# Performance work log

Hardware: AMD Instinct MI355X
Metric: run time of the kernel (lower is better)

## Reference

```python
import jax, jax.numpy as jnp
import numpy as np

K, B, S, D, V, H = 4, 64, 50, 256, 40000, 4
DH = D // H
TOPK = 2
NEG = -1e9
SCALE = float(1.0 / np.sqrt(DH))


def setup_inputs() -> dict:
    key = jax.random.key(0)
    ks = jax.random.split(key, 16)
    s = 0.05
    return {
        "ids":   jax.random.randint(ks[0], (K, B, S), 0, V),
        "items": jax.random.randint(ks[1], (K, B, S), 0, V),
        "adj":   jax.random.randint(ks[2], (B, S, S), 0, 5),
        "alias": jax.random.randint(ks[3], (B, S), 0, S),
        "eps":   jax.random.normal(ks[4], (B, S, K), jnp.float32),
        "emb":   jax.random.normal(ks[5], (K, V, D), jnp.float32) * s,
        "agg_a": jax.random.normal(ks[6], (K, 4, D), jnp.float32) * s,
        "Wq": jax.random.normal(ks[7], (K, D, D), jnp.float32) * s,
        "Wk": jax.random.normal(ks[8], (K, D, D), jnp.float32) * s,
        "Wv": jax.random.normal(ks[9], (K, D, D), jnp.float32) * s,
        "Wo": jax.random.normal(ks[10], (K, D, D), jnp.float32) * s,
        "ln1_g": jnp.ones((K, D), jnp.float32),
        "ln1_b": jnp.zeros((K, D), jnp.float32),
        "W1": jax.random.normal(ks[11], (K, D, 4 * D), jnp.float32) * s,
        "W2": jax.random.normal(ks[12], (K, 4 * D, D), jnp.float32) * s,
        "ln2_g": jnp.ones((K, D), jnp.float32),
        "ln2_b": jnp.zeros((K, D), jnp.float32),
        "Wg": jax.random.normal(ks[13], (D, K), jnp.float32) * s,
        "Wn": jax.random.normal(ks[14], (D, K), jnp.float32) * s,
    }


def _layer_norm(x, g, b):
    m = jnp.mean(x, -1, keepdims=True)
    v = jnp.var(x, -1, keepdims=True)
    return (x - m) * jax.lax.rsqrt(v + 1e-5) * g + b


def _per_key(ids, items, emb, a, Wq, Wk, Wv, Wo, g1, b1, W1, W2, g2, b2, adj, alias):
    hg = emb[items]                                          # [B,S,D] graph-node embeddings
    # LocalAggregator: relation-typed pairwise attention over session graph (adj in {1..4})
    e = jnp.einsum('bid,bjd,rd->rbij', hg, hg, a)            # [4,B,S,S], avoids [B,S,S,D]
    e = jax.nn.leaky_relu(e, 0.2)
    alpha = jnp.full(adj.shape, NEG, e.dtype)
    for r in range(4):
        alpha = jnp.where(adj == r + 1, e[r], alpha)
    alpha = jax.nn.softmax(alpha, -1)
    h_local = jnp.einsum('bij,bjd->bid', alpha, hg)          # graph aggregation
    h = jnp.take_along_axis(h_local, alias[..., None], axis=1)   # distribute graph rows to sequence
    # memory-transformer block (pre-LN causal MHA + FFN)
    x = _layer_norm(h, g1, b1)
    q = (x @ Wq).reshape(B, S, H, DH)
    k = (x @ Wk).reshape(B, S, H, DH)
    v = (x @ Wv).reshape(B, S, H, DH)
    scores = jnp.einsum('bihd,bjhd->bhij', q, k) * SCALE
    causal = jnp.tril(jnp.ones((S, S), bool))
    scores = jnp.where(causal, scores, NEG)
    attn = jax.nn.softmax(scores, -1)
    o = jnp.einsum('bhij,bjhd->bihd', attn, v).reshape(B, S, D) @ Wo
    h = h + o
    y = _layer_norm(h, g2, b2)
    h = h + jax.nn.gelu(y @ W1) @ W2
    return h


def reference(ids, items, adj, alias, eps, emb, agg_a, Wq, Wk, Wv, Wo,
              ln1_g, ln1_b, W1, W2, ln2_g, ln2_b, Wg, Wn):
    per_key = jax.vmap(_per_key, in_axes=(0,) * 14 + (None, None))
    h_keys = per_key(ids, items, emb, agg_a, Wq, Wk, Wv, Wo,
                     ln1_g, ln1_b, W1, W2, ln2_g, ln2_b, adj, alias)   # [K,B,S,D]
    # gate input: mean over per-key input-sequence embeddings (h_seq in original)
    h_seq = jax.vmap(lambda e, i: e[i])(emb, ids).mean(0)              # [B,S,D]
    # noisy top-k gating over node-type experts
    logits = h_seq @ Wg + jax.nn.softplus(h_seq @ Wn) * eps            # [B,S,K]
    top_v, top_i = jax.lax.top_k(logits, TOPK)
    w = jax.nn.softmax(top_v, -1)                                      # [B,S,TOPK]
    gates = jnp.sum(jax.nn.one_hot(top_i, K, dtype=w.dtype) * w[..., None], axis=-2)  # [B,S,K]
    return jnp.einsum('bsk,kbsd->bsd', gates, h_keys)
```

## Files before the change

kernel.cpp:

```cpp
#include <hip/hip_runtime.h>
#include <hip/hip_bf16.h>
#include <math.h>

#define K_ 4
#define B_ 64
#define S_ 50
#define D_ 256
#define V_ 40000
#define H_ 4
#define DH_ 64
#define NEG_ (-1e9f)
#define SCALE_ 0.125f

typedef __attribute__((ext_vector_type(8))) __bf16 bf16x8v;
typedef __attribute__((ext_vector_type(4))) float f32x4v;

__device__ __forceinline__ float wred_sum(float v) {
#pragma unroll
  for (int off = 32; off > 0; off >>= 1) v += __shfl_xor(v, off, 64);
  return v;
}
__device__ __forceinline__ float wred_max(float v) {
#pragma unroll
  for (int off = 32; off > 0; off >>= 1) v = fmaxf(v, __shfl_xor(v, off, 64));
  return v;
}
__device__ __forceinline__ float softplusf(float x) {
  return (x > 20.f) ? x : log1pf(expf(x));
}
__device__ __forceinline__ float geluf(float x) {
  const float c = 0.7978845608028654f;
  float x3 = x * x * x;
  return 0.5f * x * (1.f + tanhf(c * (x + 0.044715f * x3)));
}
__device__ __forceinline__ float bf2f(unsigned int u) {
  return __uint_as_float(u << 16);
}
__device__ __forceinline__ unsigned short f2bf(float f) {
  unsigned u = __float_as_uint(f);
  return (unsigned short)((u + 0x7fffu + ((u >> 16) & 1u)) >> 16);
}
__device__ __forceinline__ void unp8(uint4 a, float* d) {
  d[0] = bf2f(a.x & 0xffffu); d[1] = bf2f(a.x >> 16);
  d[2] = bf2f(a.y & 0xffffu); d[3] = bf2f(a.y >> 16);
  d[4] = bf2f(a.z & 0xffffu); d[5] = bf2f(a.z >> 16);
  d[6] = bf2f(a.w & 0xffffu); d[7] = bf2f(a.w >> 16);
}
__device__ __forceinline__ bf16x8v cvt8(float4 a, float4 b) {
  bf16x8v r;
  r[0] = (__bf16)a.x; r[1] = (__bf16)a.y; r[2] = (__bf16)a.z; r[3] = (__bf16)a.w;
  r[4] = (__bf16)b.x; r[5] = (__bf16)b.y; r[6] = (__bf16)b.z; r[7] = (__bf16)b.w;
  return r;
}

__global__ __launch_bounds__(256) void front_kernel(
    const int* __restrict__ items, const int* __restrict__ adj,
    const float* __restrict__ emb, const float* __restrict__ agg_a,
    const int* __restrict__ alias_, float* __restrict__ hbuf,
    unsigned short* __restrict__ xb,
    const float* __restrict__ ln1g, const float* __restrict__ ln1b,
    const int* __restrict__ ids, const float* __restrict__ Wg,
    const float* __restrict__ Wn, const float* __restrict__ eps,
    float* __restrict__ gates,
    const float* __restrict__ wq, const float* __restrict__ wk,
    const float* __restrict__ wv, const float* __restrict__ wo,
    const float* __restrict__ w1, const float* __restrict__ w2,
    unsigned short* __restrict__ wqkvT, unsigned short* __restrict__ woT,
    unsigned short* __restrict__ w1T, unsigned short* __restrict__ w2T) {
  __shared__ __align__(16) char smem[62816];
  int bid = blockIdx.x;
  int t = threadIdx.x;

  if (bid < 256) {
    typedef __bf16 (*arr264)[264];
    arr264 hgb = (arr264)smem;
    float (*e_f)[68] = (float(*)[68])(smem + 33792);
    unsigned char (*adj_s)[64] = (unsigned char(*)[64])(smem + 47392);
    arr264 a_sb = (arr264)(smem + 51488);
    __bf16 (*alp)[72] = (__bf16(*)[72])(smem + 53600);
    float* hl = (float*)smem;

    int kb = bid;
    int k = kb >> 6, b = kb & 63;
    for (int c = t; c < 2048; c += 256) {
      int row = c >> 5, c8 = (c & 31) * 8;
      bf16x8v val;
      if (row < S_) {
        int g = items[kb * S_ + row];
        const float* src = emb + ((long)k * V_ + g) * D_ + c8;
        val = cvt8(*(const float4*)src, *(const float4*)(src + 4));
      } else {
#pragma unroll
        for (int e = 0; e < 8; ++e) val[e] = (__bf16)0.f;
      }
      *(bf16x8v*)&hgb[row][c8] = val;
    }
    if (t < 128) {
      int row = t >> 5, c8 = (t & 31) * 8;
      const float* src = agg_a + ((long)k * 4 + row) * D_ + c8;
      *(bf16x8v*)&a_sb[row][c8] = cvt8(*(const float4*)src, *(const float4*)(src + 4));
    }
    for (int c = t; c < 4096; c += 256) {
      int i = c >> 6, j = c & 63;
      adj_s[i][j] = (i < S_ && j < S_)
                        ? (unsigned char)adj[((long)b * S_ + i) * S_ + j] : 0;
    }
    __syncthreads();
    int w = t >> 6, lane = t & 63;
    int m16 = lane & 15, quad = lane >> 4;
    float e_sel[4][4];
#pragma unroll
    for (int nt = 0; nt < 4; ++nt)
#pragma unroll
      for (int rg = 0; rg < 4; ++rg) e_sel[nt][rg] = NEG_;
#pragma unroll
    for (int r = 0; r < 4; ++r) {
      f32x4v acc[4];
#pragma unroll
      for (int nt = 0; nt < 4; ++nt) acc[nt] = (f32x4v){0.f, 0.f, 0.f, 0.f};
#pragma unroll
      for (int k0 = 0; k0 < 8; ++k0) {
        int kc = k0 * 32 + quad * 8;
        bf16x8v hr = *(const bf16x8v*)&hgb[w * 16 + m16][kc];
        bf16x8v ar = *(const bf16x8v*)&a_sb[r][kc];
        bf16x8v af;
#pragma unroll
        for (int e = 0; e < 8; ++e) af[e] = (__bf16)((float)hr[e] * (float)ar[e]);
#pragma unroll
        for (int nt = 0; nt < 4; ++nt) {
          bf16x8v bf = *(const bf16x8v*)&hgb[nt * 16 + m16][kc];
          acc[nt] = __builtin_amdgcn_mfma_f32_16x16x32_bf16(af, bf, acc[nt], 0, 0, 0);
        }
      }
#pragma unroll
      for (int nt = 0; nt < 4; ++nt)
#pragma unroll
        for (int rg = 0; rg < 4; ++rg) {
          int i = w * 16 + quad * 4 + rg, j = nt * 16 + m16;
          if (adj_s[i][j] == r + 1) {
            float v = acc[nt][rg];
            e_sel[nt][rg] = (v >= 0.f) ? v : 0.2f * v;
          }
        }
    }
#pragma unroll
    for (int nt = 0; nt < 4; ++nt)
#pragma unroll
      for (int rg = 0; rg < 4; ++rg) {
        int i = w * 16 + quad * 4 + rg;
        if (i < S_) e_f[i][nt * 16 + m16] = e_sel[nt][rg];
      }
    __syncthreads();
    for (int i = w; i < S_; i += 4) {
      float val = (lane < S_) ? e_f[i][lane] : -INFINITY;
      float m = wred_max(val);
      float p = expf(val - m);
      float ssum = wred_sum(p);
      alp[i][lane] = (__bf16)(p / ssum);
    }
    __syncthreads();
    f32x4v acc16[16];
#pragma unroll
    for (int nt = 0; nt < 16; ++nt) {
      f32x4v acc = (f32x4v){0.f, 0.f, 0.f, 0.f};
#pragma unroll
      for (int k0 = 0; k0 < 2; ++k0) {
        int jb = k0 * 32 + quad * 8;
        bf16x8v af = *(const bf16x8v*)&alp[w * 16 + m16][jb];
        bf16x8v bf;
#pragma unroll
        for (int tt = 0; tt < 8; ++tt) bf[tt] = hgb[jb + tt][nt * 16 + m16];
        acc = __builtin_amdgcn_mfma_f32_16x16x32_bf16(af, bf, acc, 0, 0, 0);
      }
      acc16[nt] = acc;
    }
    __syncthreads();
#pragma unroll
    for (int nt = 0; nt < 16; ++nt)
#pragma unroll
      for (int rg = 0; rg < 4; ++rg) {
        int i = w * 16 + quad * 4 + rg;
        if (i < S_) hl[i * 260 + nt * 16 + m16] = acc16[nt][rg];
      }
    __syncthreads();
    for (int s = w; s < S_; s += 4) {
      int src = alias_[b * S_ + s];
      const float4 v = *(const float4*)&hl[src * 260 + lane * 4];
      long off = ((long)kb * S_ + s) * D_ + lane * 4;
      *(float4*)(hbuf + off) = v;
      float sum = wred_sum(v.x + v.y + v.z + v.w);
      float sq = wred_sum(v.x * v.x + v.y * v.y + v.z * v.z + v.w * v.w);
      float mean = sum * (1.f / D_);
      float var = sq * (1.f / D_) - mean * mean;
      float rs = rsqrtf(var + 1e-5f);
      const float4 gv = *(const float4*)(ln1g + k * D_ + lane * 4);
      const float4 bv = *(const float4*)(ln1b + k * D_ + lane * 4);
      ushort4 o;
      o.x = f2bf((v.x - mean) * rs * gv.x + bv.x);
      o.y = f2bf((v.y - mean) * rs * gv.y + bv.y);
      o.z = f2bf((v.z - mean) * rs * gv.z + bv.z);
      o.w = f2bf((v.w - mean) * rs * gv.w + bv.w);
      *(ushort4*)(xb + off) = o;
    }
    return;
  }

  if (bid < 1024) {
    int tid = bid - 256;
    typedef unsigned short row66[66];
    row66* tile = (row66*)smem;
    const float* src; unsigned short* dst; int C, R; int r0, c0;
    if (tid < 192) {
      int sect = tid >> 6; int rem = tid & 63;
      int k = rem >> 4, t2 = rem & 15;
      r0 = (t2 >> 2) * 64; c0 = (t2 & 3) * 64;
      src = ((sect == 0) ? wq : (sect == 1) ? wk : wv) + (long)k * 65536;
      dst = wqkvT + ((long)k * 768 + sect * 256) * 256;
      R = 256; C = 256;
    } else if (tid < 256) {
      int rem = tid - 192; int k = rem >> 4, t2 = rem & 15;
      r0 = (t2 >> 2) * 64; c0 = (t2 & 3) * 64;
      src = wo + (long)k * 65536; dst = woT + (long)k * 65536;
      R = 256; C = 256;
    } else if (tid < 512) {
      int rem = tid - 256; int k = rem >> 6, t2 = rem & 63;
      r0 = (t2 >> 4) * 64; c0 = (t2 & 15) * 64;
      src = w1 + (long)k * 262144; dst = w1T + (long)k * 262144;
      R = 256; C = 1024;
    } else {
      int rem = tid - 512; int k = rem >> 6, t2 = rem & 63;
      r0 = (t2 >> 2) * 64; c0 = (t2 & 3) * 64;
      src = w2 + (long)k * 262144; dst = w2T + (long)k * 262144;
      R = 1024; C = 256;
    }
    int sr = t >> 2, sc = (t & 3) * 16;
    const float* p = src + (long)(r0 + sr) * C + c0 + sc;
#pragma unroll
    for (int q = 0; q < 4; ++q) {
      float4 f = *(const float4*)(p + q * 4);
      tile[sr][sc + q * 4 + 0] = f2bf(f.x);
      tile[sr][sc + q * 4 + 1] = f2bf(f.y);
      tile[sr][sc + q * 4 + 2] = f2bf(f.z);
      tile[sr][sc + q * 4 + 3] = f2bf(f.w);
    }
    __syncthreads();
    int dc = t >> 2, ch = (t & 3) * 16;
    unsigned int wds[8];
#pragma unroll
    for (int i = 0; i < 8; ++i)
      wds[i] = (unsigned int)tile[ch + 2 * i][dc] |
               ((unsigned int)tile[ch + 2 * i + 1][dc] << 16);
    unsigned short* dp = dst + (long)(c0 + dc) * R + r0 + ch;
    uint4 o0 = make_uint4(wds[0], wds[1], wds[2], wds[3]);
    uint4 o1 = make_uint4(wds[4], wds[5], wds[6], wds[7]);
    *(uint4*)dp = o0;
    *(uint4*)(dp + 8) = o1;
    return;
  }

  {
    int w = t >> 6, lane = t & 63;
    int item = (bid - 1024) * 4 + w;
    int b = item / S_, s = item % S_;
    int d0 = lane * 4;
    float4 hs = make_float4(0.f, 0.f, 0.f, 0.f);
#pragma unroll
    for (int k = 0; k < K_; ++k) {
      int id = ids[(k * B_ + b) * S_ + s];
      const float4 e = *(const float4*)(emb + ((long)k * V_ + id) * D_ + d0);
      hs.x += e.x; hs.y += e.y; hs.z += e.z; hs.w += e.w;
    }
    hs.x *= 0.25f; hs.y *= 0.25f; hs.z *= 0.25f; hs.w *= 0.25f;
    float logit[4];
#pragma unroll
    for (int j = 0; j < K_; ++j) {
      float pg = hs.x * Wg[(d0 + 0) * K_ + j] + hs.y * Wg[(d0 + 1) * K_ + j] +
                 hs.z * Wg[(d0 + 2) * K_ + j] + hs.w * Wg[(d0 + 3) * K_ + j];
      float pn = hs.x * Wn[(d0 + 0) * K_ + j] + hs.y * Wn[(d0 + 1) * K_ + j] +
                 hs.z * Wn[(d0 + 2) * K_ + j] + hs.w * Wn[(d0 + 3) * K_ + j];
      pg = wred_sum(pg);
      pn = wred_sum(pn);
      logit[j] = pg + softplusf(pn) * eps[item * K_ + j];
    }
    if (lane == 0) {
      int i0 = 0; float v0 = logit[0];
      for (int j = 1; j < K_; ++j) if (logit[j] > v0) { v0 = logit[j]; i0 = j; }
      int i1 = -1; float v1 = 0.f;
      for (int j = 0; j < K_; ++j)
        if (j != i0 && (i1 < 0 || logit[j] > v1)) { v1 = logit[j]; i1 = j; }
      float w0 = 1.f / (1.f + expf(v1 - v0));
      float w1 = 1.f - w0;
#pragma unroll
      for (int j = 0; j < K_; ++j)
        gates[item * K_ + j] = (j == i0) ? w0 : ((j == i1) ? w1 : 0.f);
    }
  }
}

__global__ __launch_bounds__(256) void bgemm3(
    const unsigned short* __restrict__ A, const unsigned short* __restrict__ Bt,
    long strideA, long strideBt, int N, int Kd,
    unsigned short* __restrict__ Cb, long strideCb, int act) {
  __shared__ unsigned short sA[128][72];
  __shared__ unsigned short sB[128][72];
  int z = blockIdx.z;
  A += (long)z * strideA;
  Bt += (long)z * strideBt;
  int t = threadIdx.x, w = t >> 6, lane = t & 63;
  int wr = w >> 1, wc = w & 1;
  int row0 = blockIdx.y * 128, col0 = blockIdx.x * 128;
  int m16 = lane & 15, quad = lane >> 4;
  f32x4v acc[4][4];
#pragma unroll
  for (int mr = 0; mr < 4; ++mr)
#pragma unroll
    for (int nr = 0; nr < 4; ++nr) acc[mr][nr] = (f32x4v){0.f, 0.f, 0.f, 0.f};
  int sr = t >> 1, sc = (t & 1) * 32;
  const unsigned short* pa = A + (long)(row0 + sr) * Kd + sc;
  const unsigned short* pb = Bt + (long)(col0 + sr) * Kd + sc;
  uint4 a0 = *(const uint4*)(pa);
  uint4 a1 = *(const uint4*)(pa + 8);
  uint4 a2 = *(const uint4*)(pa + 16);
  uint4 a3 = *(const uint4*)(pa + 24);
  uint4 b0 = *(const uint4*)(pb);
  uint4 b1 = *(const uint4*)(pb + 8);
  uint4 b2 = *(const uint4*)(pb + 16);
  uint4 b3 = *(const uint4*)(pb + 24);
  for (int k0 = 0; k0 < Kd; k0 += 64) {
    __syncthreads();
    *(uint4*)&sA[sr][sc] = a0;
    *(uint4*)&sA[sr][sc + 8] = a1;
    *(uint4*)&sA[sr][sc + 16] = a2;
    *(uint4*)&sA[sr][sc + 24] = a3;
    *(uint4*)&sB[sr][sc] = b0;
    *(uint4*)&sB[sr][sc + 8] = b1;
    *(uint4*)&sB[sr][sc + 16] = b2;
    *(uint4*)&sB[sr][sc + 24] = b3;
    if (k0 + 64 < Kd) {
      a0 = *(const uint4*)(pa + k0 + 64);
      a1 = *(const uint4*)(pa + k0 + 72);
      a2 = *(const uint4*)(pa + k0 + 80);
      a3 = *(const uint4*)(pa + k0 + 88);
      b0 = *(const uint4*)(pb + k0 + 64);
      b1 = *(const uint4*)(pb + k0 + 72);
      b2 = *(const uint4*)(pb + k0 + 80);
      b3 = *(const uint4*)(pb + k0 + 88);
    }
    __syncthreads();
#pragma unroll
    for (int half = 0; half < 2; ++half) {
      int kg = half * 32 + quad * 8;
      bf16x8v af[4], bf[4];
#pragma unroll
      for (int i = 0; i < 4; ++i) {
        af[i] = *(const bf16x8v*)&sA[wr * 64 + i * 16 + m16][kg];
        bf[i] = *(const bf16x8v*)&sB[wc * 64 + i * 16 + m16][kg];
      }
#pragma unroll
      for (int mr = 0; mr < 4; ++mr)
#pragma unroll
        for (int nr = 0; nr < 4; ++nr)
          acc[mr][nr] = __builtin_amdgcn_mfma_f32_16x16x32_bf16(
              af[mr], bf[nr], acc[mr][nr], 0, 0, 0);
    }
  }
#pragma unroll
  for (int mr = 0; mr < 4; ++mr) {
    int rbase = row0 + wr * 64 + mr * 16 + quad * 4;
#pragma unroll
    for (int nr = 0; nr < 4; ++nr) {
      int col = col0 + wc * 64 + nr * 16 + m16;
#pragma unroll
      for (int i2 = 0; i2 < 4; ++i2) {
        float vv = acc[mr][nr][i2];
        if (act == 1) vv = geluf(vv);
        Cb[(long)z * strideCb + (long)(rbase + i2) * N + col] = f2bf(vv);
      }
    }
  }
}

__global__ __launch_bounds__(256) void attn_kernel(
    const unsigned short* __restrict__ qkv, unsigned short* __restrict__ o) {
  __shared__ float qs[S_][65], ks[S_][65], vs[S_][65];
  int idx = blockIdx.x;
  int h = idx & 3;
  int kb = idx >> 2;
  long base = (long)kb * S_ * 768;
  int t = threadIdx.x;
  for (int f = t; f < S_ * 8; f += 256) {
    int row = f >> 3, c8 = (f & 7) * 8;
    long g = base + (long)row * 768 + h * DH_ + c8;
    unp8(*(const uint4*)(qkv + g), &qs[row][c8]);
    unp8(*(const uint4*)(qkv + g + 256), &ks[row][c8]);
    unp8(*(const uint4*)(qkv + g + 512), &vs[row][c8]);
  }
  __syncthreads();
  int w = t >> 6, lane = t & 63;
  for (int i = w; i < S_; i += 4) {
    int jj = (lane < S_) ? lane : 0;
    float dot = 0.f;
#pragma unroll
    for (int d = 0; d < DH_; ++d) dot = fmaf(qs[i][d], ks[jj][d], dot);
    float val = (lane <= i) ? dot * SCALE_ : ((lane < S_) ? NEG_ : -INFINITY);
    float m = wred_max(val);
    float p = expf(val - m);
    float ssum = wred_sum(p);
    float pr = p / ssum;
    float acc = 0.f;
    for (int j = 0; j <= i; ++j)
      acc = fmaf(__shfl(pr, j, 64), vs[j][lane], acc);
    o[((long)kb * S_ + i) * D_ + h * DH_ + lane] = f2bf(acc);
  }
}

__global__ __launch_bounds__(256) void bgemm_oln(
    const unsigned short* __restrict__ A, const unsigned short* __restrict__ Bt,
    float* __restrict__ hbuf, unsigned short* __restrict__ y,
    const float* __restrict__ g2, const float* __restrict__ b2) {
  __shared__ unsigned short sA[64][72];
  __shared__ unsigned short sB[256][72];
  const long BSD = (long)B_ * S_ * D_;
  int z = blockIdx.z;
  const unsigned short* Ap = A + (long)z * BSD;
  const unsigned short* Bp = Bt + (long)z * 65536;
  int t = threadIdx.x, w = t >> 6, lane = t & 63;
  int row0 = blockIdx.x * 64;
  int m16 = lane & 15, quad = lane >> 4;
  f32x4v acc[16];
#pragma unroll
  for (int nt = 0; nt < 16; ++nt) acc[nt] = (f32x4v){0.f, 0.f, 0.f, 0.f};
  int sr = t >> 2, sc = (t & 3) * 16;
  const unsigned short* pa = Ap + (long)(row0 + sr) * 256 + sc;
  const unsigned short* pb = Bp + (long)sr * 256 + sc;
  uint4 a0 = *(const uint4*)pa;
  uint4 a1 = *(const uint4*)(pa + 8);
  uint4 bv[8];
#pragma unroll
  for (int q = 0; q < 4; ++q) {
    bv[2 * q] = *(const uint4*)(pb + q * 16384);
    bv[2 * q + 1] = *(const uint4*)(pb + q * 16384 + 8);
  }
  for (int k0 = 0; k0 < 256; k0 += 64) {
    __syncthreads();
    *(uint4*)&sA[sr][sc] = a0;
    *(uint4*)&sA[sr][sc + 8] = a1;
#pragma unroll
    for (int q = 0; q < 4; ++q) {
      *(uint4*)&sB[q * 64 + sr][sc] = bv[2 * q];
      *(uint4*)&sB[q * 64 + sr][sc + 8] = bv[2 * q + 1];
    }
    if (k0 + 64 < 256) {
      a0 = *(const uint4*)(pa + k0 + 64);
      a1 = *(const uint4*)(pa + k0 + 72);
#pragma unroll
      for (int q = 0; q < 4; ++q) {
        bv[2 * q] = *(const uint4*)(pb + q * 16384 + k0 + 64);
        bv[2 * q + 1] = *(const uint4*)(pb + q * 16384 + k0 + 72);
      }
    }
    __syncthreads();
#pragma unroll
    for (int half = 0; half < 2; ++half) {
      int kg = half * 32 + quad * 8;
      bf16x8v af = *(const bf16x8v*)&sA[w * 16 + m16][kg];
#pragma unroll
      for (int nt = 0; nt < 16; ++nt) {
        bf16x8v bf = *(const bf16x8v*)&sB[nt * 16 + m16][kg];
        acc[nt] = __builtin_amdgcn_mfma_f32_16x16x32_bf16(af, bf, acc[nt], 0, 0, 0);
      }
    }
  }
  long zoff = (long)z * BSD;
  int rbase = row0 + w * 16 + quad * 4;
#pragma unroll
  for (int nt = 0; nt < 16; ++nt)
#pragma unroll
    for (int i2 = 0; i2 < 4; ++i2) {
      long off = zoff + (long)(rbase + i2) * 256 + nt * 16 + m16;
      float vv = acc[nt][i2] + hbuf[off];
      acc[nt][i2] = vv;
      hbuf[off] = vv;
    }
  float mean[4], rstd[4];
#pragma unroll
  for (int i2 = 0; i2 < 4; ++i2) {
    float s = 0.f, q = 0.f;
#pragma unroll
    for (int nt = 0; nt < 16; ++nt) {
      float vv = acc[nt][i2];
      s += vv; q += vv * vv;
    }
#pragma unroll
    for (int off = 1; off < 16; off <<= 1) {
      s += __shfl_xor(s, off, 64);
      q += __shfl_xor(q, off, 64);
    }
    float m = s * (1.f / D_);
    float var = q * (1.f / D_) - m * m;
    mean[i2] = m;
    rstd[i2] = rsqrtf(var + 1e-5f);
  }
#pragma unroll
  for (int nt = 0; nt < 16; ++nt) {
    float gv = g2[z * D_ + nt * 16 + m16];
    float bvv = b2[z * D_ + nt * 16 + m16];
#pragma unroll
    for (int i2 = 0; i2 < 4; ++i2) {
      long off = zoff + (long)(rbase + i2) * 256 + nt * 16 + m16;
      y[off] = f2bf((acc[nt][i2] - mean[i2]) * rstd[i2] * gv + bvv);
    }
  }
}

__global__ __launch_bounds__(256) void bgemm_f2a(
    const unsigned short* __restrict__ A, const unsigned short* __restrict__ Bt,
    const float* __restrict__ hbuf, const float* __restrict__ gates,
    float* __restrict__ out) {
  __shared__ unsigned short sA[64][72];
  __shared__ unsigned short sB[64][72];
  const long T4 = 3276800;
  const long BSD = (long)B_ * S_ * D_;
  int z = blockIdx.z;
  int t = threadIdx.x, w = t >> 6, lane = t & 63;
  int col0 = blockIdx.x * 64, row0 = blockIdx.y * 64;
  int m16 = lane & 15, quad = lane >> 4;
  f32x4v acc[4];
#pragma unroll
  for (int nt = 0; nt < 4; ++nt) acc[nt] = (f32x4v){0.f, 0.f, 0.f, 0.f};
  int sr = t >> 2, sc = (t & 3) * 16;
  const unsigned short* pa = A + (long)z * T4 + (long)(row0 + sr) * 1024 + sc;
  const unsigned short* pb = Bt + (long)z * 262144 + (long)(col0 + sr) * 1024 + sc;
  uint4 a0 = *(const uint4*)pa;
  uint4 a1 = *(const uint4*)(pa + 8);
  uint4 b0 = *(const uint4*)pb;
  uint4 b1 = *(const uint4*)(pb + 8);
  for (int k0 = 0; k0 < 1024; k0 += 64) {
    __syncthreads();
    *(uint4*)&sA[sr][sc] = a0;
    *(uint4*)&sA[sr][sc + 8] = a1;
    *(uint4*)&sB[sr][sc] = b0;
    *(uint4*)&sB[sr][sc + 8] = b1;
    if (k0 + 64 < 1024) {
      a0 = *(const uint4*)(pa + k0 + 64);
      a1 = *(const uint4*)(pa + k0 + 72);
      b0 = *(const uint4*)(pb + k0 + 64);
      b1 = *(const uint4*)(pb + k0 + 72);
    }
    __syncthreads();
#pragma unroll
    for (int half = 0; half < 2; ++half) {
      int kg = half * 32 + quad * 8;
      bf16x8v af = *(const bf16x8v*)&sA[w * 16 + m16][kg];
#pragma unroll
      for (int nt = 0; nt < 4; ++nt) {
        bf16x8v bf = *(const bf16x8v*)&sB[nt * 16 + m16][kg];
        acc[nt] = __builtin_amdgcn_mfma_f32_16x16x32_bf16(af, bf, acc[nt], 0, 0, 0);
      }
    }
  }
  int rbase = row0 + w * 16 + quad * 4;
#pragma unroll
  for (int i2 = 0; i2 < 4; ++i2) {
    float gz = gates[(rbase + i2) * 4 + z];
    if (gz != 0.f) {
#pragma unroll
      for (int nt = 0; nt < 4; ++nt) {
        long off = (long)(rbase + i2) * 256 + col0 + nt * 16 + m16;
        float vv = gz * (acc[nt][i2] + hbuf[(long)z * BSD + off]);
        atomicAdd(&out[off], vv);
      }
    }
  }
}

extern "C" void kernel_launch(void* const* d_in, const int* in_sizes, int n_in,
                              void* d_out, int out_size, void* d_ws,
                              size_t ws_size, hipStream_t stream) {
  const int* ids = (const int*)d_in[0];
  const int* items = (const int*)d_in[1];
  const int* adj = (const int*)d_in[2];
  const int* alias = (const int*)d_in[3];
  const float* eps = (const float*)d_in[4];
  const float* emb = (const float*)d_in[5];
  const float* agg_a = (const float*)d_in[6];
  const float* Wq = (const float*)d_in[7];
  const float* Wk = (const float*)d_in[8];
  const float* Wv = (const float*)d_in[9];
  const float* Wo = (const float*)d_in[10];
  const float* ln1g = (const float*)d_in[11];
  const float* ln1b = (const float*)d_in[12];
  const float* W1 = (const float*)d_in[13];
  const float* W2 = (const float*)d_in[14];
  const float* ln2g = (const float*)d_in[15];
  const float* ln2b = (const float*)d_in[16];
  const float* Wg = (const float*)d_in[17];
  const float* Wn = (const float*)d_in[18];
  float* out = (float*)d_out;

  const long BSD = (long)B_ * S_ * D_;
  float* ws = (float*)d_ws;
  float* gates = ws;
  float* hbuf = ws + 16384;
  unsigned short* ub = (unsigned short*)(ws + 16384 + 4 * BSD);
  unsigned short* xb = ub;
  unsigned short* qkvb = ub + 3276800;
  unsigned short* tb = qkvb;
  unsigned short* wqkvT = ub + 16384000;
  unsigned short* woT = wqkvT + 786432;
  unsigned short* w1T = woT + 262144;
  unsigned short* w2T = w1T + 1048576;

  const long T4 = 3276800;

  hipMemsetAsync(out, 0, (size_t)BSD * sizeof(float), stream);

  front_kernel<<<1824, 256, 0, stream>>>(
      items, adj, emb, agg_a, alias, hbuf, xb, ln1g, ln1b,
      ids, Wg, Wn, eps, gates,
      Wq, Wk, Wv, Wo, W1, W2, wqkvT, woT, w1T, w2T);
  bgemm3<<<dim3(6, 25, 4), 256, 0, stream>>>(xb, wqkvT, BSD, 196608, 768, 256,
      qkvb, 2457600, 0);
  attn_kernel<<<K_ * B_ * H_, 256, 0, stream>>>(qkvb, xb);
  bgemm_oln<<<dim3(50, 1, 4), 256, 0, stream>>>(xb, woT, hbuf, xb, ln2g, ln2b);
  bgemm3<<<dim3(8, 25, 4), 256, 0, stream>>>(xb, w1T, BSD, 262144, 1024, 256,
      tb, T4, 1);
  bgemm_f2a<<<dim3(4, 50, 4), 256, 0, stream>>>(tb, w2T, hbuf, gates, out);
}
```

Measured before the change: 429.5 us.

## Rewrite causal self-attention kernel to use bf16 MFMA for QK and PV

Replaces the scalar per-row attention kernel with one that keeps Q, K and V in shared memory as bf16 padded to 64 rows. QK^T and P·V are computed with 16x16x32 bf16 MFMA instructions, and the softmax is done in registers with 16-lane shuffles. Probabilities are split into hi/lo bf16 parts to keep accuracy, which doubles the PV MFMAs. The intent is to remove the serial FMA loops and shuffle-driven PV accumulation. The V operand is gathered column-wise from LDS, which may cause bank conflicts.

Result: faster. 398.0 us (-7.3%).

```diff
diff --git a/kernel.cpp b/kernel.cpp
--- a/kernel.cpp
+++ b/kernel.cpp
@@ -39,12 +39,6 @@
 __device__ __forceinline__ unsigned short f2bf(float f) {
   unsigned u = __float_as_uint(f);
   return (unsigned short)((u + 0x7fffu + ((u >> 16) & 1u)) >> 16);
-}
-__device__ __forceinline__ void unp8(uint4 a, float* d) {
-  d[0] = bf2f(a.x & 0xffffu); d[1] = bf2f(a.x >> 16);
-  d[2] = bf2f(a.y & 0xffffu); d[3] = bf2f(a.y >> 16);
-  d[4] = bf2f(a.z & 0xffffu); d[5] = bf2f(a.z >> 16);
-  d[6] = bf2f(a.w & 0xffffu); d[7] = bf2f(a.w >> 16);
 }
 __device__ __forceinline__ bf16x8v cvt8(float4 a, float4 b) {
   bf16x8v r;
@@ -380,38 +374,108 @@
   }
 }
 
-__global__ __launch_bounds__(256) void attn_kernel(
+__global__ __launch_bounds__(256) void attn_mfma(
     const unsigned short* __restrict__ qkv, unsigned short* __restrict__ o) {
-  __shared__ float qs[S_][65], ks[S_][65], vs[S_][65];
+  __shared__ __bf16 qs[64][72], ks[64][72], vs[64][72];
+  __shared__ __bf16 psh[64][72], psl[64][72];
   int idx = blockIdx.x;
   int h = idx & 3;
   int kb = idx >> 2;
-  long base = (long)kb * S_ * 768;
+  long base = (long)kb * S_ * 768 + h * DH_;
   int t = threadIdx.x;
-  for (int f = t; f < S_ * 8; f += 256) {
+  for (int f = t; f < 512; f += 256) {
     int row = f >> 3, c8 = (f & 7) * 8;
-    long g = base + (long)row * 768 + h * DH_ + c8;
-    unp8(*(const uint4*)(qkv + g), &qs[row][c8]);
-    unp8(*(const uint4*)(qkv + g + 256), &ks[row][c8]);
-    unp8(*(const uint4*)(qkv + g + 512), &vs[row][c8]);
+    uint4 zq = make_uint4(0, 0, 0, 0), zk = zq, zv = zq;
+    if (row < S_) {
+      long g = base + (long)row * 768 + c8;
+      zq = *(const uint4*)(qkv + g);
+      zk = *(const uint4*)(qkv + g + 256);
+      zv = *(const uint4*)(qkv + g + 512);
+    }
+    *(uint4*)&qs[row][c8] = zq;
+    *(uint4*)&ks[row][c8] = zk;
+    *(uint4*)&vs[row][c8] = zv;
   }
   __syncthreads();
   int w = t >> 6, lane = t & 63;
-  for (int i = w; i < S_; i += 4) {
-    int jj = (lane < S_) ? lane : 0;
-    float dot = 0.f;
-#pragma unroll
-    for (int d = 0; d < DH_; ++d) dot = fmaf(qs[i][d], ks[jj][d], dot);
-    float val = (lane <= i) ? dot * SCALE_ : ((lane < S_) ? NEG_ : -INFINITY);
-    float m = wred_max(val);
-    float p = expf(val - m);
-    float ssum = wred_sum(p);
-    float pr = p / ssum;
-    float acc = 0.f;
-    for (int j = 0; j <= i; ++j)
-      acc = fmaf(__shfl(pr, j, 64), vs[j][lane], acc);
-    o[((long)kb * S_ + i) * D_ + h * DH_ + lane] = f2bf(acc);
-  }
+  int m16 = lane & 15, quad = lane >> 4;
+  f32x4v sacc[4];
+#pragma unroll
+  for (int nt = 0; nt < 4; ++nt) sacc[nt] = (f32x4v){0.f, 0.f, 0.f, 0.f};
+#pragma unroll
+  for (int k0 = 0; k0 < 2; ++k0) {
+    int kc = k0 * 32 + quad * 8;
+    bf16x8v af = *(const bf16x8v*)&qs[w * 16 + m16][kc];
+#pragma unroll
+    for (int nt = 0; nt < 4; ++nt) {
+      bf16x8v bf = *(const bf16x8v*)&ks[nt * 16 + m16][kc];
+      sacc[nt] = __builtin_amdgcn_mfma_f32_16x16x32_bf16(af, bf, sacc[nt], 0, 0, 0);
+    }
+  }
+#pragma unroll
+  for (int rg = 0; rg < 4; ++rg) {
+    int i = w * 16 + quad * 4 + rg;
+    float v4[4];
+    if (i < S_) {
+      float mx = -INFINITY;
+#pragma unroll
+      for (int nt = 0; nt < 4; ++nt) {
+        int j = nt * 16 + m16;
+        float vv = (j <= i) ? sacc[nt][rg] * SCALE_ : -INFINITY;
+        v4[nt] = vv;
+        mx = fmaxf(mx, vv);
+      }
+#pragma unroll
+      for (int off = 1; off < 16; off <<= 1)
+        mx = fmaxf(mx, __shfl_xor(mx, off, 64));
+      float sum = 0.f;
+#pragma unroll
+      for (int nt = 0; nt < 4; ++nt) {
+        v4[nt] = expf(v4[nt] - mx);
+        sum += v4[nt];
+      }
+#pragma unroll
+      for (int off = 1; off < 16; off <<= 1) sum += __shfl_xor(sum, off, 64);
+      float inv = 1.f / sum;
+#pragma unroll
+      for (int nt = 0; nt < 4; ++nt) v4[nt] *= inv;
+    } else {
+#pragma unroll
+      for (int nt = 0; nt < 4; ++nt) v4[nt] = 0.f;
+    }
+#pragma unroll
+    for (int nt = 0; nt < 4; ++nt) {
+      __bf16 hi = (__bf16)v4[nt];
+      psh[i][nt * 16 + m16] = hi;
+      psl[i][nt * 16 + m16] = (__bf16)(v4[nt] - (float)hi);
+    }
+  }
+  __syncthreads();
+  f32x4v oacc[4];
+#pragma unroll
+  for (int nt = 0; nt < 4; ++nt) oacc[nt] = (f32x4v){0.f, 0.f, 0.f, 0.f};
+#pragma unroll
+  for (int k0 = 0; k0 < 2; ++k0) {
+    int jb = k0 * 32 + quad * 8;
+    bf16x8v ah = *(const bf16x8v*)&psh[w * 16 + m16][jb];
+    bf16x8v al = *(const bf16x8v*)&psl[w * 16 + m16][jb];
+#pragma unroll
+    for (int nt = 0; nt < 4; ++nt) {
+      bf16x8v bf;
+#pragma unroll
+      for (int tt = 0; tt < 8; ++tt) bf[tt] = vs[jb + tt][nt * 16 + m16];
+      oacc[nt] = __builtin_amdgcn_mfma_f32_16x16x32_bf16(ah, bf, oacc[nt], 0, 0, 0);
+      oacc[nt] = __builtin_amdgcn_mfma_f32_16x16x32_bf16(al, bf, oacc[nt], 0, 0, 0);
+    }
+  }
+#pragma unroll
+  for (int nt = 0; nt < 4; ++nt)
+#pragma unroll
+    for (int rg = 0; rg < 4; ++rg) {
+      int i = w * 16 + quad * 4 + rg;
+      if (i < S_)
+        o[((long)kb * S_ + i) * D_ + h * DH_ + nt * 16 + m16] = f2bf(oacc[nt][rg]);
+    }
 }
 
 __global__ __launch_bounds__(256) void bgemm_oln(
@@ -621,7 +685,7 @@
       Wq, Wk, Wv, Wo, W1, W2, wqkvT, woT, w1T, w2T);
   bgemm3<<<dim3(6, 25, 4), 256, 0, stream>>>(xb, wqkvT, BSD, 196608, 768, 256,
       qkvb, 2457600, 0);
-  attn_kernel<<<K_ * B_ * H_, 256, 0, stream>>>(qkvb, xb);
+  attn_mfma<<<K_ * B_ * H_, 256, 0, stream>>>(qkvb, xb);
   bgemm_oln<<<dim3(50, 1, 4), 256, 0, stream>>>(xb, woT, hbuf, xb, ln2g, ln2b);
   bgemm3<<<dim3(8, 25, 4), 256, 0, stream>>>(xb, w1T, BSD, 262144, 1024, 256,
       tb, T4, 1);
```
